# Optimization experiments

Hardware: AMD Instinct MI355X
Metric: run time of the kernel (lower is better)

The kernel has to match this reference:

```python
import jax, jax.numpy as jnp
import numpy as np

WINDOW_SIZE = 11
SIGMA = 1.5
C1 = 0.01 ** 2
C2 = 0.03 ** 2


def _gaussian_window(window_size=WINDOW_SIZE, sigma=SIGMA):
    x = np.arange(window_size)
    g = np.exp(-((x - window_size // 2) ** 2) / float(2 * sigma ** 2))
    g = g / g.sum()
    w2d = np.outer(g, g).astype(np.float32)
    # OIHW layout: [out_ch=1, in_ch=1, K, K]
    return jnp.asarray(w2d)[None, None, :, :]


def _conv_same(x, window):
    # x: [B,1,H,W], window: [1,1,K,K]; depthwise conv with 1 channel == plain conv
    pad = WINDOW_SIZE // 2
    return jax.lax.conv_general_dilated(
        x, window,
        window_strides=(1, 1),
        padding=((pad, pad), (pad, pad)),
        dimension_numbers=("NCHW", "OIHW", "NCHW"),
    )


def setup_inputs() -> dict:
    key = jax.random.key(0)
    k1, k2 = jax.random.split(key)
    B, C, H, W = 128, 1, 256, 256
    img1 = jax.random.uniform(k1, (B, C, H, W), dtype=jnp.float32)
    img2 = jax.random.uniform(k2, (B, C, H, W), dtype=jnp.float32)
    return {"img1": img1, "img2": img2}


def reference(img1, img2):
    window = _gaussian_window().astype(img1.dtype)
    mu1 = _conv_same(img1, window)
    mu2 = _conv_same(img2, window)
    mu1_sq = mu1 * mu1
    mu2_sq = mu2 * mu2
    mu1_mu2 = mu1 * mu2
    sigma1_sq = _conv_same(img1 * img1, window) - mu1_sq
    sigma2_sq = _conv_same(img2 * img2, window) - mu2_sq
    sigma12 = _conv_same(img1 * img2, window) - mu1_mu2
    ssim_map = ((2 * mu1_mu2 + C1) * (2 * sigma12 + C2)) / (
        (mu1_sq + mu2_sq + C1) * (sigma1_sq + sigma2_sq + C2)
    )
    return 1 - jnp.mean(ssim_map)
```

## Files before the change

### kernel.cpp

```cpp
#include <hip/hip_runtime.h>


#define IMG_W 256
#define IMG_H 256
#define N_PIX (128.0f * 256.0f * 256.0f)

__global__ void ssim_init(float* out) { out[0] = 1.0f; }

__global__ __launch_bounds__(256) void ssim_main(
    const float* __restrict__ img1, const float* __restrict__ img2,
    float* __restrict__ out) {
  const float WK[11] = {0.00102838f, 0.00759873f, 0.03600077f, 0.10936070f,
                        0.21300543f, 0.26601173f, 0.21300543f, 0.10936070f,
                        0.03600077f, 0.00759873f, 0.00102838f};

  __shared__ float2 stage[4][2][128];
  __shared__ float wsum[4];

  const int tid = threadIdx.x;
  const int lane = tid & 63;
  const int wid = tid >> 6;
  const int gw = __builtin_amdgcn_readfirstlane(blockIdx.x * 4 + wid);
  const int img = gw >> 5;
  const int rem = gw & 31;
  const int rs = (rem >> 2) << 5;
  const int cs = (rem & 3) << 6;
  const int r0 = rs - 5;
  const char* q1 = (const char*)(img1 + (size_t)img * (IMG_W * IMG_H));
  const char* q2 = (const char*)(img2 + (size_t)img * (IMG_W * IMG_H));

  const int c0 = cs - 8 + lane;
  const int c1 = c0 + 64;
  const float cm0 = (c0 >= 0) ? 1.0f : 0.0f;
  const float cm1 = (c1 < IMG_W) ? 1.0f : 0.0f;
  const int co0 = (c0 < 0 ? 0 : c0) * 4;
  const int co1 = (c1 > IMG_W - 1 ? IMG_W - 1 : c1) * 4;

#define ROWOFF(ri) (((ri) < 0 ? 0 : ((ri) > IMG_H - 1 ? IMG_H - 1 : (ri))) << 10)
#define LOADROW(ri, X0, Y0, X1, Y1)                  \
  {                                                  \
    const int ro_ = ROWOFF(ri);                      \
    const int o0_ = ro_ + co0, o1_ = ro_ + co1;      \
    X0 = *(const float*)(q1 + o0_) * cm0;            \
    Y0 = *(const float*)(q2 + o0_) * cm0;            \
    X1 = *(const float*)(q1 + o1_) * cm1;            \
    Y1 = *(const float*)(q2 + o1_) * cm1;            \
  }

  float rx[11], ry[11], rxx[11], ryy[11], rxy[11];
  float acc = 0.f;

  float x0, y0, x1, y1;
  {
    float a0, b0, a1, b1;
    LOADROW(r0, a0, b0, a1, b1);
    stage[wid][0][lane] = make_float2(a0, b0);
    stage[wid][0][64 + lane] = make_float2(a1, b1);
    LOADROW(r0 + 1, x0, y0, x1, y1);
  }

  for (int bl = 0; bl < 44; bl += 11) {
#pragma unroll
    for (int u = 0; u < 11; ++u) {
      const int li = bl + u;
      if (li < 42) {
        const int ri = r0 + li;
        float nx0 = 0.f, ny0 = 0.f, nx1 = 0.f, ny1 = 0.f;
        if (li + 2 < 42) LOADROW(ri + 2, nx0, ny0, nx1, ny1);
        if (li + 1 < 42) {
          float2* wb = &stage[wid][(li + 1) & 1][0];
          wb[lane] = make_float2(x0, y0);
          wb[64 + lane] = make_float2(x1, y1);
        }
        {
          const float2* rbuf = &stage[wid][li & 1][0];
          float sx = 0.f, sy = 0.f, sxx = 0.f, syy = 0.f, sxy = 0.f;
#pragma unroll
          for (int k = 0; k < 11; ++k) {
            const float2 v = rbuf[lane + 3 + k];
            const float wk = WK[k];
            const float tx = wk * v.x;
            const float ty = wk * v.y;
            sx += tx;
            sy += ty;
            sxx = fmaf(tx, v.x, sxx);
            syy = fmaf(ty, v.y, syy);
            sxy = fmaf(tx, v.y, sxy);
          }
          if (ri >= 0 && ri < IMG_H) {
            rx[u] = sx; ry[u] = sy; rxx[u] = sxx; ryy[u] = syy; rxy[u] = sxy;
          } else {
            rx[u] = 0.f; ry[u] = 0.f; rxx[u] = 0.f; ryy[u] = 0.f; rxy[u] = 0.f;
          }
        }
        if (li >= 10) {
          float m1 = 0.f, m2 = 0.f, e11 = 0.f, e22 = 0.f, e12 = 0.f;
#pragma unroll
          for (int j = 0; j < 11; ++j) {
            const int s = (u + 1 + j) % 11;
            const float wj = WK[j];
            m1 = fmaf(wj, rx[s], m1);
            m2 = fmaf(wj, ry[s], m2);
            e11 = fmaf(wj, rxx[s], e11);
            e22 = fmaf(wj, ryy[s], e22);
            e12 = fmaf(wj, rxy[s], e12);
          }
          const float C1 = 1e-4f, C2 = 9e-4f;
          const float mu11 = m1 * m1, mu22 = m2 * m2, mu12 = m1 * m2;
          const float s11 = e11 - mu11, s22 = e22 - mu22, s12 = e12 - mu12;
          const float num = (2.f * mu12 + C1) * (2.f * s12 + C2);
          const float den = (mu11 + mu22 + C1) * (s11 + s22 + C2);
          float rcp = __builtin_amdgcn_rcpf(den);
          rcp = rcp * fmaf(-den, rcp, 2.0f);
          acc = fmaf(num, rcp, acc);
        }
        x0 = nx0; y0 = ny0; x1 = nx1; y1 = ny1;
      }
    }
  }

  acc += __shfl_down(acc, 32);
  acc += __shfl_down(acc, 16);
  acc += __shfl_down(acc, 8);
  acc += __shfl_down(acc, 4);
  acc += __shfl_down(acc, 2);
  acc += __shfl_down(acc, 1);
  if (lane == 0) wsum[wid] = acc;
  __syncthreads();
  if (tid == 0) {
    const float s = wsum[0] + wsum[1] + wsum[2] + wsum[3];
    atomicAdd(out, s * (-1.0f / N_PIX));
  }
}

extern "C" void kernel_launch(void* const* d_in, const int* in_sizes, int n_in,
                              void* d_out, int out_size, void* d_ws,
                              size_t ws_size, hipStream_t stream) {
  const float* img1 = (const float*)d_in[0];
  const float* img2 = (const float*)d_in[1];
  float* out = (float*)d_out;
  ssim_init<<<1, 1, 0, stream>>>(out);
  ssim_main<<<1024, 256, 0, stream>>>(img1, img2, out);
}
```

Measured before the change: 120.5 us.

## Process row pairs with packed float2 math and one-wave blocks

Each wave now handles two image rows per step, storing x and y in separate LDS arrays and doing the horizontal and vertical passes with packed two-wide FMAs (v_pk_fma) across the row pair. The vertical ring buffer shrinks from 11 to 8 slots of paired rows, and the vertical filter is split into two packed accumulations with scalar tail terms. Blocks become single 64-thread waves, 4096 of them, with a 3-waves occupancy hint and a per-wave atomic in place of the block-level LDS reduction. The aim is to halve VALU instruction count through packed math and to drop the __syncthreads. The cost is four times as many atomics on the output and higher register pressure.

After: 224.7 us. 86.5% more time.

```diff
diff --git a/kernel.cpp b/kernel.cpp
--- a/kernel.cpp
+++ b/kernel.cpp
@@ -1,136 +1,154 @@
 #include <hip/hip_runtime.h>
 
+
+typedef float f32x2 __attribute__((ext_vector_type(2)));
 
 #define IMG_W 256
 #define IMG_H 256
 #define N_PIX (128.0f * 256.0f * 256.0f)
+#define NPAIR 22
+
+static __device__ __forceinline__ f32x2 fma2(f32x2 a, f32x2 b, f32x2 c) {
+  return __builtin_elementwise_fma(a, b, c);
+}
 
 __global__ void ssim_init(float* out) { out[0] = 1.0f; }
 
-__global__ __launch_bounds__(256) void ssim_main(
+__global__ __launch_bounds__(64, 3) void ssim_main(
     const float* __restrict__ img1, const float* __restrict__ img2,
     float* __restrict__ out) {
-  const float WK[11] = {0.00102838f, 0.00759873f, 0.03600077f, 0.10936070f,
-                        0.21300543f, 0.26601173f, 0.21300543f, 0.10936070f,
-                        0.03600077f, 0.00759873f, 0.00102838f};
+  const float W0 = 0.00102838f, W1 = 0.00759873f, W2 = 0.03600077f,
+              W3 = 0.10936070f, W4 = 0.21300543f, W5 = 0.26601173f,
+              W6 = 0.21300543f, W7 = 0.10936070f, W8 = 0.03600077f,
+              W9 = 0.00759873f, W10 = 0.00102838f;
+  const float WH[11] = {W0, W1, W2, W3, W4, W5, W6, W7, W8, W9, W10};
+  const f32x2 CV0[5] = {{W1, W2}, {W3, W4}, {W5, W6}, {W7, W8}, {W9, W10}};
+  const f32x2 CV1[5] = {{W0, W1}, {W2, W3}, {W4, W5}, {W6, W7}, {W8, W9}};
 
-  __shared__ float2 stage[4][2][128];
-  __shared__ float wsum[4];
+  __shared__ f32x2 LSX[2][128];
+  __shared__ f32x2 LSY[2][128];
 
-  const int tid = threadIdx.x;
-  const int lane = tid & 63;
-  const int wid = tid >> 6;
-  const int gw = __builtin_amdgcn_readfirstlane(blockIdx.x * 4 + wid);
+  const int lane = threadIdx.x;
+  const int gw = blockIdx.x;
   const int img = gw >> 5;
   const int rem = gw & 31;
   const int rs = (rem >> 2) << 5;
   const int cs = (rem & 3) << 6;
-  const int r0 = rs - 5;
+  const int r0p = rs - 6;
   const char* q1 = (const char*)(img1 + (size_t)img * (IMG_W * IMG_H));
   const char* q2 = (const char*)(img2 + (size_t)img * (IMG_W * IMG_H));
 
   const int c0 = cs - 8 + lane;
   const int c1 = c0 + 64;
-  const float cm0 = (c0 >= 0) ? 1.0f : 0.0f;
-  const float cm1 = (c1 < IMG_W) ? 1.0f : 0.0f;
-  const int co0 = (c0 < 0 ? 0 : c0) * 4;
-  const int co1 = (c1 > IMG_W - 1 ? IMG_W - 1 : c1) * 4;
+  const float cm0 = (c0 >= 0) ? 1.f : 0.f;
+  const float cm1 = (c1 < IMG_W) ? 1.f : 0.f;
+  const int co0 = (c0 < 0 ? 0 : c0) << 2;
+  const int co1 = (c1 > IMG_W - 1 ? IMG_W - 1 : c1) << 2;
+  const f32x2 vm0 = {cm0, cm0};
+  const f32x2 vm1 = {cm1, cm1};
 
-#define ROWOFF(ri) (((ri) < 0 ? 0 : ((ri) > IMG_H - 1 ? IMG_H - 1 : (ri))) << 10)
-#define LOADROW(ri, X0, Y0, X1, Y1)                  \
-  {                                                  \
-    const int ro_ = ROWOFF(ri);                      \
-    const int o0_ = ro_ + co0, o1_ = ro_ + co1;      \
-    X0 = *(const float*)(q1 + o0_) * cm0;            \
-    Y0 = *(const float*)(q2 + o0_) * cm0;            \
-    X1 = *(const float*)(q1 + o1_) * cm1;            \
-    Y1 = *(const float*)(q2 + o1_) * cm1;            \
+#define CLAMPR(r) ((r) < 0 ? 0 : ((r) > IMG_H - 1 ? IMG_H - 1 : (r)))
+#define PAIRLOAD(P, X0, Y0, X1, Y1)                                           \
+  do {                                                                        \
+    const int ra_ = r0p + 2 * (P), rb_ = ra_ + 1;                             \
+    const char* a1_ = q1 + (CLAMPR(ra_) << 10);                               \
+    const char* b1_ = q1 + (CLAMPR(rb_) << 10);                               \
+    const char* a2_ = q2 + (CLAMPR(ra_) << 10);                               \
+    const char* b2_ = q2 + (CLAMPR(rb_) << 10);                               \
+    X0 = (f32x2){*(const float*)(a1_ + co0), *(const float*)(b1_ + co0)} * vm0; \
+    Y0 = (f32x2){*(const float*)(a2_ + co0), *(const float*)(b2_ + co0)} * vm0; \
+    X1 = (f32x2){*(const float*)(a1_ + co1), *(const float*)(b1_ + co1)} * vm1; \
+    Y1 = (f32x2){*(const float*)(a2_ + co1), *(const float*)(b2_ + co1)} * vm1; \
+  } while (0)
+
+  f32x2 rS1[8], rS2[8], rS11[8], rS22[8], rS12[8];
+  f32x2 accv = {0.f, 0.f};
+
+  f32x2 hx0, hy0, hx1, hy1, nx0, ny0, nx1, ny1;
+  PAIRLOAD(0, hx0, hy0, hx1, hy1);
+  LSX[0][lane] = hx0; LSY[0][lane] = hy0;
+  LSX[0][64 + lane] = hx1; LSY[0][64 + lane] = hy1;
+  PAIRLOAD(1, hx0, hy0, hx1, hy1);
+
+#pragma unroll
+  for (int li = 0; li < NPAIR; ++li) {
+    if (li + 2 < NPAIR) PAIRLOAD(li + 2, nx0, ny0, nx1, ny1);
+    if (li + 1 < NPAIR) {
+      const int b = (li + 1) & 1;
+      LSX[b][lane] = hx0; LSY[b][lane] = hy0;
+      LSX[b][64 + lane] = hx1; LSY[b][64 + lane] = hy1;
+    }
+    {
+      const f32x2* bx = &LSX[li & 1][lane];
+      const f32x2* by = &LSY[li & 1][lane];
+      f32x2 s1 = {0, 0}, s2 = {0, 0}, s11 = {0, 0}, s22 = {0, 0}, s12 = {0, 0};
+#pragma unroll
+      for (int k = 0; k < 11; ++k) {
+        const f32x2 vx = bx[3 + k];
+        const f32x2 vy = by[3 + k];
+        const f32x2 tx = vx * WH[k];
+        const f32x2 ty = vy * WH[k];
+        s1 += tx; s2 += ty;
+        s11 = fma2(tx, vx, s11);
+        s22 = fma2(ty, vy, s22);
+        s12 = fma2(tx, vy, s12);
+      }
+      const int ra = r0p + 2 * li;
+      const float vr = ((unsigned)ra < IMG_H) ? 1.f : 0.f;
+      const f32x2 vmr = {vr, vr};
+      rS1[li & 7] = s1 * vmr; rS2[li & 7] = s2 * vmr;
+      rS11[li & 7] = s11 * vmr; rS22[li & 7] = s22 * vmr;
+      rS12[li & 7] = s12 * vmr;
+    }
+    if (li >= 6) {
+#define SLm(m) ((li + 2 + (m)) & 7)
+#define VERT(R, V0, V1)                              \
+  do {                                               \
+    f32x2 a0_ = R[SLm(1)] * CV0[0];                  \
+    a0_ = fma2(CV0[1], R[SLm(2)], a0_);              \
+    a0_ = fma2(CV0[2], R[SLm(3)], a0_);              \
+    a0_ = fma2(CV0[3], R[SLm(4)], a0_);              \
+    a0_ = fma2(CV0[4], R[SLm(5)], a0_);              \
+    V0 = fmaf(W0, R[SLm(0)].y, a0_.x + a0_.y);       \
+    f32x2 a1_ = R[SLm(1)] * CV1[0];                  \
+    a1_ = fma2(CV1[1], R[SLm(2)], a1_);              \
+    a1_ = fma2(CV1[2], R[SLm(3)], a1_);              \
+    a1_ = fma2(CV1[3], R[SLm(4)], a1_);              \
+    a1_ = fma2(CV1[4], R[SLm(5)], a1_);              \
+    V1 = fmaf(W10, R[SLm(6)].x, a1_.x + a1_.y);      \
+  } while (0)
+      float m1a, m1b, m2a, m2b, e11a, e11b, e22a, e22b, e12a, e12b;
+      VERT(rS1, m1a, m1b);
+      VERT(rS2, m2a, m2b);
+      VERT(rS11, e11a, e11b);
+      VERT(rS22, e22a, e22b);
+      VERT(rS12, e12a, e12b);
+      const f32x2 m1 = {m1a, m1b}, m2 = {m2a, m2b};
+      const f32x2 e11 = {e11a, e11b}, e22 = {e22a, e22b}, e12 = {e12a, e12b};
+      const f32x2 c1v = {1e-4f, 1e-4f}, c2v = {9e-4f, 9e-4f};
+      const f32x2 mu11 = m1 * m1, mu22 = m2 * m2, mu12 = m1 * m2;
+      const f32x2 sg11 = e11 - mu11, sg22 = e22 - mu22, sg12 = e12 - mu12;
+      const f32x2 num = (mu12 * 2.0f + c1v) * (sg12 * 2.0f + c2v);
+      const f32x2 den = (mu11 + mu22 + c1v) * (sg11 + sg22 + c2v);
+      float t0 = __builtin_amdgcn_rcpf(den.x);
+      t0 = t0 * fmaf(-den.x, t0, 2.f);
+      float t1 = __builtin_amdgcn_rcpf(den.y);
+      t1 = t1 * fmaf(-den.y, t1, 2.f);
+      accv = fma2(num, (f32x2){t0, t1}, accv);
+#undef VERT
+#undef SLm
+    }
+    hx0 = nx0; hy0 = ny0; hx1 = nx1; hy1 = ny1;
   }
 
-  float rx[11], ry[11], rxx[11], ryy[11], rxy[11];
-  float acc = 0.f;
-
-  float x0, y0, x1, y1;
-  {
-    float a0, b0, a1, b1;
-    LOADROW(r0, a0, b0, a1, b1);
-    stage[wid][0][lane] = make_float2(a0, b0);
-    stage[wid][0][64 + lane] = make_float2(a1, b1);
-    LOADROW(r0 + 1, x0, y0, x1, y1);
-  }
-
-  for (int bl = 0; bl < 44; bl += 11) {
-#pragma unroll
-    for (int u = 0; u < 11; ++u) {
-      const int li = bl + u;
-      if (li < 42) {
-        const int ri = r0 + li;
-        float nx0 = 0.f, ny0 = 0.f, nx1 = 0.f, ny1 = 0.f;
-        if (li + 2 < 42) LOADROW(ri + 2, nx0, ny0, nx1, ny1);
-        if (li + 1 < 42) {
-          float2* wb = &stage[wid][(li + 1) & 1][0];
-          wb[lane] = make_float2(x0, y0);
-          wb[64 + lane] = make_float2(x1, y1);
-        }
-        {
-          const float2* rbuf = &stage[wid][li & 1][0];
-          float sx = 0.f, sy = 0.f, sxx = 0.f, syy = 0.f, sxy = 0.f;
-#pragma unroll
-          for (int k = 0; k < 11; ++k) {
-            const float2 v = rbuf[lane + 3 + k];
-            const float wk = WK[k];
-            const float tx = wk * v.x;
-            const float ty = wk * v.y;
-            sx += tx;
-            sy += ty;
-            sxx = fmaf(tx, v.x, sxx);
-            syy = fmaf(ty, v.y, syy);
-            sxy = fmaf(tx, v.y, sxy);
-          }
-          if (ri >= 0 && ri < IMG_H) {
-            rx[u] = sx; ry[u] = sy; rxx[u] = sxx; ryy[u] = syy; rxy[u] = sxy;
-          } else {
-            rx[u] = 0.f; ry[u] = 0.f; rxx[u] = 0.f; ryy[u] = 0.f; rxy[u] = 0.f;
-          }
-        }
-        if (li >= 10) {
-          float m1 = 0.f, m2 = 0.f, e11 = 0.f, e22 = 0.f, e12 = 0.f;
-#pragma unroll
-          for (int j = 0; j < 11; ++j) {
-            const int s = (u + 1 + j) % 11;
-            const float wj = WK[j];
-            m1 = fmaf(wj, rx[s], m1);
-            m2 = fmaf(wj, ry[s], m2);
-            e11 = fmaf(wj, rxx[s], e11);
-            e22 = fmaf(wj, ryy[s], e22);
-            e12 = fmaf(wj, rxy[s], e12);
-          }
-          const float C1 = 1e-4f, C2 = 9e-4f;
-          const float mu11 = m1 * m1, mu22 = m2 * m2, mu12 = m1 * m2;
-          const float s11 = e11 - mu11, s22 = e22 - mu22, s12 = e12 - mu12;
-          const float num = (2.f * mu12 + C1) * (2.f * s12 + C2);
-          const float den = (mu11 + mu22 + C1) * (s11 + s22 + C2);
-          float rcp = __builtin_amdgcn_rcpf(den);
-          rcp = rcp * fmaf(-den, rcp, 2.0f);
-          acc = fmaf(num, rcp, acc);
-        }
-        x0 = nx0; y0 = ny0; x1 = nx1; y1 = ny1;
-      }
-    }
-  }
-
-  acc += __shfl_down(acc, 32);
-  acc += __shfl_down(acc, 16);
-  acc += __shfl_down(acc, 8);
-  acc += __shfl_down(acc, 4);
-  acc += __shfl_down(acc, 2);
-  acc += __shfl_down(acc, 1);
-  if (lane == 0) wsum[wid] = acc;
-  __syncthreads();
-  if (tid == 0) {
-    const float s = wsum[0] + wsum[1] + wsum[2] + wsum[3];
-    atomicAdd(out, s * (-1.0f / N_PIX));
-  }
+  float tot = accv.x + accv.y;
+  tot += __shfl_xor(tot, 1);
+  tot += __shfl_xor(tot, 2);
+  tot += __shfl_xor(tot, 4);
+  tot += __shfl_xor(tot, 8);
+  tot += __shfl_xor(tot, 16);
+  tot += __shfl_xor(tot, 32);
+  if (lane == 0) atomicAdd(out, tot * (-1.0f / N_PIX));
 }
 
 extern "C" void kernel_launch(void* const* d_in, const int* in_sizes, int n_in,
@@ -140,5 +158,5 @@
   const float* img2 = (const float*)d_in[1];
   float* out = (float*)d_out;
   ssim_init<<<1, 1, 0, stream>>>(out);
-  ssim_main<<<1024, 256, 0, stream>>>(img1, img2, out);
+  ssim_main<<<4096, 64, 0, stream>>>(img1, img2, out);
 }
```
